# Kernel optimization log

Measured on AMD Instinct MI355X. Metric: run time of the kernel, lower is better.

## Reference

```python
import jax, jax.numpy as jnp
import numpy as np

B, N, NODE, EDGE, H, SK, SV, PK, PV = 1, 512, 256, 128, 8, 16, 16, 4, 4
EPS = 1e-8
SCALAR_SCALE = (3 * SK) ** -0.5          # num_attn_logits=3
POINT_SCALE = (3 * PK * (9.0 / 2.0)) ** -0.5
PAIR_SCALE = 3 ** -0.5


def setup_inputs() -> dict:
    key = jax.random.key(0)
    ks = jax.random.split(key, 16)
    s = 0.02
    return {
        "node": jax.random.normal(ks[0], (B, N, NODE), jnp.float32),
        "edge": jax.random.normal(ks[1], (B, N, N, EDGE), jnp.float32),
        "rotations": jax.random.normal(ks[2], (B, N, 3, 3), jnp.float32),
        "translations": jax.random.normal(ks[3], (B, N, 3), jnp.float32),
        "W_sq": jax.random.normal(ks[4], (NODE, H * SK), jnp.float32) * s,
        "W_sk": jax.random.normal(ks[5], (NODE, H * SK), jnp.float32) * s,
        "W_sv": jax.random.normal(ks[6], (NODE, H * SV), jnp.float32) * s,
        "W_pq": jax.random.normal(ks[7], (NODE, H * PK * 3), jnp.float32) * s,
        "W_pk": jax.random.normal(ks[8], (NODE, H * PK * 3), jnp.float32) * s,
        "W_pv": jax.random.normal(ks[9], (NODE, H * PV * 3), jnp.float32) * s,
        "point_weights": jnp.log(jnp.expm1(jnp.ones((H,), jnp.float32))),  # softplus^-1(1)
        "W_pb": jax.random.normal(ks[10], (EDGE, H), jnp.float32) * s,
        "b_pb": jnp.zeros((H,), jnp.float32),
        "W_out": jax.random.normal(ks[11], (H * (SV + EDGE + PV * 4), NODE), jnp.float32) * s,
        "b_out": jnp.zeros((NODE,), jnp.float32),
    }


def reference(node, edge, rotations, translations, W_sq, W_sk, W_sv, W_pq, W_pk, W_pv,
              point_weights, W_pb, b_pb, W_out, b_out):
    b, n, _ = node.shape
    # scalar q/k/v: (b, n, h, d)
    qs = (node @ W_sq).reshape(b, n, H, SK)
    ks_ = (node @ W_sk).reshape(b, n, H, SK)
    vs = (node @ W_sv).reshape(b, n, H, SV)
    # point q/k/v in local frame: (b, n, h, d, 3) -> rotate + translate into global frame
    t = translations[:, :, None, None, :]  # (b, n, 1, 1, 3)
    qp = jnp.einsum('bnhdc,bnrc->bnhdr', (node @ W_pq).reshape(b, n, H, PK, 3), rotations) + t
    kp = jnp.einsum('bnhdc,bnrc->bnhdr', (node @ W_pk).reshape(b, n, H, PK, 3), rotations) + t
    vp = jnp.einsum('bnhdc,bnrc->bnhdr', (node @ W_pv).reshape(b, n, H, PV, 3), rotations) + t

    # scalar logits (b, h, i, j)
    logits_scalar = jnp.einsum('bihd,bjhd->bhij', qs, ks_) * SCALAR_SCALE
    # pairwise bias (b, h, i, j)
    logits_pair = (jnp.einsum('bijd,dh->bhij', edge, W_pb) + b_pb[None, :, None, None]) * PAIR_SCALE
    # point logits: sum_{d,c} ||q - k||^2 via expansion (avoids (b,i,j,h,d,3) tensor)
    q2 = (qp ** 2).sum((-2, -1)).transpose(0, 2, 1)  # (b, h, i)
    k2 = (kp ** 2).sum((-2, -1)).transpose(0, 2, 1)  # (b, h, j)
    cross = jnp.einsum('bihdc,bjhdc->bhij', qp, kp)
    point_dist = q2[:, :, :, None] + k2[:, :, None, :] - 2.0 * cross  # (b, h, i, j)
    pw = jax.nn.softplus(point_weights)[None, :, None, None]  # (1, h, 1, 1)
    logits_points = -0.5 * (point_dist * pw * POINT_SCALE)

    attn = jax.nn.softmax(logits_scalar + logits_points + logits_pair, axis=-1)  # (b, h, i, j)

    res_scalar = jnp.einsum('bhij,bjhd->bihd', attn, vs).reshape(b, n, H * SV)
    res_pair = jnp.einsum('bhij,bijd->bihd', attn, edge).reshape(b, n, H * EDGE)
    res_pts = jnp.einsum('bhij,bjhdr->bihdr', attn, vp) - t  # back to origin
    res_pts = jnp.einsum('bnhdr,bnrc->bnhdc', res_pts, rotations)  # inverse rotation (R^T)
    res_norm = jnp.sqrt((res_pts ** 2).sum(-1) + EPS)  # (b, n, h, d)

    out = jnp.concatenate([
        res_scalar,
        res_pts.reshape(b, n, H * PV * 3),
        res_norm.reshape(b, n, H * PV),
        res_pair,
    ], axis=-1)
    return out @ W_out + b_out
```

## Files before the change

### kernel.cpp

```cpp
#include <hip/hip_runtime.h>
#include <hip/hip_fp16.h>
#include <math.h>

#define NN 512
#define NODE_D 256
#define EDGE_D 128
#define HN 8

#define SCALAR_SCALE 0.14433756729740643f
#define POINT_SCALE  0.13608276348795434f
#define PAIR_SCALE   0.5773502691896258f

#define OFF_QS   0
#define OFF_KS   65536
#define OFF_VS   131072
#define OFF_VP   196608
#define OFF_QCAT 245760
#define OFF_KCAT 393216
#define OFF_FEAT 540672
#define OFF_PRAW OFF_FEAT
#define OFF_LG16 1196032
#define OFF_OUTP 2244608

__global__ __launch_bounds__(256) void k_projgemm(
    const float* __restrict__ node,
    const float* __restrict__ Wsq, const float* __restrict__ Wsk, const float* __restrict__ Wsv,
    const float* __restrict__ Wpq, const float* __restrict__ Wpk, const float* __restrict__ Wpv,
    float* __restrict__ ws)
{
  __shared__ float As[32 * 33];
  __shared__ float Bs[32 * 36];
  const int t = threadIdx.x;
  const int it = blockIdx.x;
  const int ct = blockIdx.y;

  const float* W; int ncol, col0; float* dst; int ldd, dcol0;
  if (ct < 12) {
    int a = ct >> 2;
    W = (a == 0) ? Wsq : (a == 1) ? Wsk : Wsv;
    ncol = 128; col0 = (ct & 3) * 32;
    dst = ws + ((a == 0) ? OFF_QS : (a == 1) ? OFF_KS : OFF_VS);
    ldd = 128; dcol0 = col0;
  } else {
    int p = ct - 12;
    int a = p / 3, cc = p % 3;
    W = (a == 0) ? Wpq : (a == 1) ? Wpk : Wpv;
    ncol = 96; col0 = cc * 32;
    dst = ws + OFF_PRAW;
    ldd = 288; dcol0 = a * 96 + cc * 32;
  }

  const int row = t & 31, cb = (t >> 5) * 4;
  float4 acc = {0.f, 0.f, 0.f, 0.f};

  for (int kt = 0; kt < 8; ++kt) {
    __syncthreads();
    #pragma unroll
    for (int q = 0; q < 4; ++q) {
      int f = t + q * 256; int r = f >> 5, c = f & 31;
      As[r * 33 + c] = node[(size_t)(it * 32 + r) * 256 + kt * 32 + c];
      Bs[r * 36 + c] = W[(size_t)(kt * 32 + r) * ncol + col0 + c];
    }
    __syncthreads();
    #pragma unroll
    for (int k = 0; k < 32; ++k) {
      float a = As[row * 33 + k];
      float4 b = *(const float4*)&Bs[k * 36 + cb];
      acc.x += a * b.x; acc.y += a * b.y; acc.z += a * b.z; acc.w += a * b.w;
    }
  }
  *(float4*)&dst[(size_t)(it * 32 + row) * ldd + dcol0 + cb] = acc;
}

__global__ __launch_bounds__(256) void k_rot2(
    const float* __restrict__ rotm, const float* __restrict__ trans,
    const float* __restrict__ pw_in, const float* __restrict__ bpb,
    float* __restrict__ ws)
{
  __shared__ float p_l[4][288];
  __shared__ float r_l[4][288];
  __shared__ float q2_l[4][8];
  __shared__ float k2_l[4][8];
  __shared__ float pw_l[8];
  __shared__ float bpb_l[8];
  const int t = threadIdx.x;
  const int n0 = blockIdx.x * 4;
  const float* praw = ws + OFF_PRAW;
  const float* qs_g = ws + OFF_QS;
  const float* ks_g = ws + OFF_KS;

  if (t < 8) {
    float x = pw_in[t];
    pw_l[t] = 0.5f * POINT_SCALE * logf(1.0f + expf(x));
    bpb_l[t] = bpb[t];
  }
  for (int idx = t; idx < 1152; idx += 256) {
    int row = idx / 288, rem = idx % 288;
    p_l[row][rem] = praw[(size_t)(n0 + row) * 288 + rem];
  }
  __syncthreads();

  for (int idx = t; idx < 1152; idx += 256) {
    int row = idx / 288, rem = idx % 288;
    int a = rem / 96, col = rem % 96;
    int rr = col % 3;
    int n = n0 + row;
    const float* R = rotm + (size_t)(n * 3 + rr) * 3;
    const float* P = &p_l[row][a * 96 + (col - rr)];
    float val = P[0] * R[0] + P[1] * R[1] + P[2] * R[2] + trans[n * 3 + rr];
    r_l[row][a * 96 + col] = val;
    if (a == 2) (ws + OFF_VP)[(size_t)n * 96 + col] = val;
  }
  __syncthreads();

  if (t < 64) {
    int row = t >> 4, rem = t & 15;
    int which = rem >> 3, h = rem & 7;
    const float* src = &r_l[row][which * 96 + h * 12];
    float s = 0.f;
    #pragma unroll
    for (int m = 0; m < 12; ++m) s += src[m] * src[m];
    if (which == 0) q2_l[row][h] = s; else k2_l[row][h] = s;
  }
  __syncthreads();

  for (int idx = t; idx < 2304; idx += 256) {
    int side = idx >= 1152;
    int per = idx - side * 1152;
    int row = per / 288, s = per % 288;
    int h = s / 36, e = s % 36;
    int n = n0 + row;
    float val;
    if (!side) {
      val = (e < 16) ? qs_g[(size_t)n * 128 + h * 16 + e] * SCALAR_SCALE
          : (e < 28) ? 2.0f * pw_l[h] * r_l[row][h * 12 + (e - 16)]
          : (e == 32) ? -pw_l[h]
          : (e == 33) ? (bpb_l[h] * PAIR_SCALE - pw_l[h] * q2_l[row][h])
          : 0.f;
      (ws + OFF_QCAT)[(size_t)n * 288 + s] = val;
    } else {
      val = (e < 16) ? ks_g[(size_t)n * 128 + h * 16 + e]
          : (e < 28) ? r_l[row][96 + h * 12 + (e - 16)]
          : (e == 32) ? k2_l[row][h]
          : (e == 33) ? 1.f
          : 0.f;
      (ws + OFF_KCAT)[(size_t)n * 288 + s] = val;
    }
  }
}

__global__ __launch_bounds__(256) void k_S(
    const float* __restrict__ ws_c, __half* __restrict__ lg16)
{
  __shared__ float4 Qt[32 * 36];
  __shared__ float4 Kt[32 * 37];
  __shared__ __half lgst[32 * 32 * 8];
  const int t = threadIdx.x;
  const int it = blockIdx.x, jt = blockIdx.y;
  const float* Qc = ws_c + OFF_QCAT;
  const float* Kc = ws_c + OFF_KCAT;
  const int ti = t >> 4, tj = t & 15;

  for (int hg = 0; hg < 2; ++hg) {
    __syncthreads();
    for (int f = t; f < 1152; f += 256) {
      int row = f / 36, c = f % 36;
      Qt[row * 36 + c] = *(const float4*)&Qc[(size_t)(it * 32 + row) * 288 + hg * 144 + c * 4];
      Kt[row * 37 + c] = *(const float4*)&Kc[(size_t)(jt * 32 + row) * 288 + hg * 144 + c * 4];
    }
    __syncthreads();

    float acc[2][2][4];
    #pragma unroll
    for (int a = 0; a < 2; ++a)
      #pragma unroll
      for (int b = 0; b < 2; ++b)
        #pragma unroll
        for (int h = 0; h < 4; ++h) acc[a][b][h] = 0.f;

    for (int c = 0; c < 9; ++c) {
      #pragma unroll
      for (int hh = 0; hh < 4; ++hh) {
        float4 q0 = Qt[(2 * ti + 0) * 36 + hh * 9 + c];
        float4 q1 = Qt[(2 * ti + 1) * 36 + hh * 9 + c];
        float4 k0 = Kt[(2 * tj + 0) * 37 + hh * 9 + c];
        float4 k1 = Kt[(2 * tj + 1) * 37 + hh * 9 + c];
        acc[0][0][hh] += q0.x * k0.x + q0.y * k0.y + q0.z * k0.z + q0.w * k0.w;
        acc[0][1][hh] += q0.x * k1.x + q0.y * k1.y + q0.z * k1.z + q0.w * k1.w;
        acc[1][0][hh] += q1.x * k0.x + q1.y * k0.y + q1.z * k0.z + q1.w * k0.w;
        acc[1][1][hh] += q1.x * k1.x + q1.y * k1.y + q1.z * k1.z + q1.w * k1.w;
      }
    }
    #pragma unroll
    for (int a = 0; a < 2; ++a)
      #pragma unroll
      for (int b = 0; b < 2; ++b)
        #pragma unroll
        for (int hh = 0; hh < 4; ++hh)
          lgst[((2 * ti + a) * 32 + (2 * tj + b)) * 8 + hg * 4 + hh] = __float2half(acc[a][b][hh]);
  }
  __syncthreads();

  for (int f = t; f < 1024; f += 256) {
    int il = f >> 5, jl = f & 31;
    float4 v = *(const float4*)&lgst[(il * 32 + jl) * 8];
    *(float4*)&lg16[((size_t)(it * 32 + il) * 512 + jt * 32 + jl) * 8] = v;
  }
}

static __device__ inline __half2 shfl_xor_h2(__half2 h, int m) {
  int v = __builtin_bit_cast(int, h);
  v = __shfl_xor(v, m);
  return __builtin_bit_cast(__half2, v);
}

__global__ __launch_bounds__(256) void k_pair(
    const float* __restrict__ edge, const float* __restrict__ Wpb,
    __half* __restrict__ lg16)
{
  const int t = threadIdx.x;
  const int jt = blockIdx.x, i = blockIdx.y;
  const int l = t & 63, w = t >> 6;
  const int rg = (l >> 4) & 3, sub = l & 15;

  float wv[4][2][8];
  #pragma unroll
  for (int k = 0; k < 4; ++k)
    #pragma unroll
    for (int c = 0; c < 2; ++c)
      #pragma unroll
      for (int h = 0; h < 8; ++h)
        wv[k][c][h] = Wpb[(size_t)(2 * sub + c + 32 * k) * 8 + h] * PAIR_SCALE;

  for (int p = 0; p < 8; ++p) {
    const int r = p * 16 + w * 4 + rg;
    const int j = jt * 128 + r;
    const float* eptr = edge + ((size_t)i * 512 + j) * 128 + 2 * sub;

    float2 e0 = *(const float2*)(eptr);
    float2 e1 = *(const float2*)(eptr + 32);
    float2 e2 = *(const float2*)(eptr + 64);
    float2 e3 = *(const float2*)(eptr + 96);

    float p8[8];
    #pragma unroll
    for (int h = 0; h < 8; ++h)
      p8[h] = e0.x * wv[0][0][h] + e0.y * wv[0][1][h]
            + e1.x * wv[1][0][h] + e1.y * wv[1][1][h]
            + e2.x * wv[2][0][h] + e2.y * wv[2][1][h]
            + e3.x * wv[3][0][h] + e3.y * wv[3][1][h];

    __half2 h0 = __floats2half2_rn(p8[0], p8[1]);
    __half2 h1 = __floats2half2_rn(p8[2], p8[3]);
    __half2 h2 = __floats2half2_rn(p8[4], p8[5]);
    __half2 h3 = __floats2half2_rn(p8[6], p8[7]);
    #pragma unroll
    for (int m = 1; m <= 8; m <<= 1) {
      h0 = __hadd2(h0, shfl_xor_h2(h0, m));
      h1 = __hadd2(h1, shfl_xor_h2(h1, m));
      h2 = __hadd2(h2, shfl_xor_h2(h2, m));
      h3 = __hadd2(h3, shfl_xor_h2(h3, m));
    }
    if (sub == 0) {
      __half* dst = lg16 + ((size_t)i * 512 + j) * 8;
      float4 cur = *(float4*)dst;
      __half2* ch = (__half2*)&cur;
      ch[0] = __hadd2(ch[0], h0);
      ch[1] = __hadd2(ch[1], h1);
      ch[2] = __hadd2(ch[2], h2);
      ch[3] = __hadd2(ch[3], h3);
      *(float4*)dst = cur;
    }
  }
}

__global__ __launch_bounds__(256) void k_attnout(
    const float* __restrict__ edge, const float* __restrict__ rotm,
    const float* __restrict__ trans, const float* __restrict__ ws,
    const __half* __restrict__ lg16, float* __restrict__ feat)
{
  __shared__ float aw[512 * 12];
  __shared__ float pl[8 * 128 * 8];
  __shared__ float vsp[8 * 128];
  __shared__ float vpp[8 * 96];
  __shared__ float op_l[96];
  __shared__ float rp_l[96];
  __shared__ float linv_l[8];

  const int t = threadIdx.x;
  const int i = blockIdx.x;

  {
    const int lane = t & 63, wid = t >> 6;
    #pragma unroll
    for (int hh = 0; hh < 2; ++hh) {
      int h = wid * 2 + hh;
      float x[8];
      float m = -1e30f;
      #pragma unroll
      for (int r = 0; r < 8; ++r) {
        int j = lane + r * 64;
        x[r] = __half2float(lg16[((size_t)i * 512 + j) * 8 + h]);
        m = fmaxf(m, x[r]);
      }
      #pragma unroll
      for (int s = 32; s; s >>= 1) m = fmaxf(m, __shfl_xor(m, s));
      float ssum = 0.f;
      #pragma unroll
      for (int r = 0; r < 8; ++r) {
        float pv = __expf(x[r] - m);
        ssum += pv;
        aw[(lane + r * 64) * 12 + h] = pv;
      }
      #pragma unroll
      for (int s = 32; s; s >>= 1) ssum += __shfl_xor(ssum, s);
      if (lane == 0) linv_l[h] = 1.0f / ssum;
    }
  }
  __syncthreads();

  const int dq = t & 31, js = t >> 5;
  const int b = dq >> 4;
  const int c0 = dq, c1 = dq + 32, c2 = dq + 64;
  const int h0 = c0 / 12, h1 = c1 / 12, h2 = c2 / 12;

  float4 aclo[4], achi[4];
  #pragma unroll
  for (int k = 0; k < 4; ++k) { aclo[k] = {0,0,0,0}; achi[k] = {0,0,0,0}; }
  float avs[4] = {0,0,0,0};
  float avp[3] = {0,0,0};

  const float* ebase = edge + (size_t)i * 512 * 128;
  const float* vsg = ws + OFF_VS;
  const float* vpg = ws + OFF_VP;

  for (int jj = 0; jj < 64; ++jj) {
    int j = js * 64 + jj;
    const float* er = ebase + (size_t)j * 128 + dq;
    const float* vr = vsg + (size_t)j * 128 + dq;
    const float* pr = vpg + (size_t)j * 96;
    float4 wlo = *(const float4*)&aw[j * 12];
    float4 whi = *(const float4*)&aw[j * 12 + 4];
    #pragma unroll
    for (int k = 0; k < 4; ++k) {
      float e = er[32 * k];
      aclo[k].x += wlo.x * e; aclo[k].y += wlo.y * e;
      aclo[k].z += wlo.z * e; aclo[k].w += wlo.w * e;
      achi[k].x += whi.x * e; achi[k].y += whi.y * e;
      achi[k].z += whi.z * e; achi[k].w += whi.w * e;
      float vv = vr[32 * k];
      float wk = (k == 0) ? (b ? wlo.y : wlo.x)
               : (k == 1) ? (b ? wlo.w : wlo.z)
               : (k == 2) ? (b ? whi.y : whi.x)
               :            (b ? whi.w : whi.z);
      avs[k] += wk * vv;
    }
    avp[0] += aw[j * 12 + h0] * pr[c0];
    avp[1] += aw[j * 12 + h1] * pr[c1];
    avp[2] += aw[j * 12 + h2] * pr[c2];
  }

  #pragma unroll
  for (int k = 0; k < 4; ++k) {
    int d = dq + 32 * k;
    *(float4*)&pl[(js * 128 + d) * 8] = aclo[k];
    *(float4*)&pl[(js * 128 + d) * 8 + 4] = achi[k];
    vsp[js * 128 + d] = avs[k];
  }
  vpp[js * 96 + c0] = avp[0];
  vpp[js * 96 + c1] = avp[1];
  vpp[js * 96 + c2] = avp[2];
  __syncthreads();

  float* frow = feat + (size_t)i * 1280;

  {
    int d = t >> 1, hq = (t & 1) * 4;
    float4 s = {0,0,0,0};
    #pragma unroll
    for (int q = 0; q < 8; ++q) {
      float4 v = *(const float4*)&pl[(q * 128 + d) * 8 + hq];
      s.x += v.x; s.y += v.y; s.z += v.z; s.w += v.w;
    }
    frow[256 + (hq + 0) * 128 + d] = s.x * linv_l[hq + 0];
    frow[256 + (hq + 1) * 128 + d] = s.y * linv_l[hq + 1];
    frow[256 + (hq + 2) * 128 + d] = s.z * linv_l[hq + 2];
    frow[256 + (hq + 3) * 128 + d] = s.w * linv_l[hq + 3];
  }
  if (t < 128) {
    float s = 0.f;
    #pragma unroll
    for (int q = 0; q < 8; ++q) s += vsp[q * 128 + t];
    frow[t] = s * linv_l[t >> 4];
  }
  if (t < 96) {
    float s = 0.f;
    #pragma unroll
    for (int q = 0; q < 8; ++q) s += vpp[q * 96 + t];
    op_l[t] = s * linv_l[t / 12] - trans[i * 3 + (t % 3)];
  }
  __syncthreads();

  if (t < 96) {
    int c = t % 3, base = t - c;
    const float* R = rotm + (size_t)i * 9;
    float val = op_l[base] * R[c] + op_l[base + 1] * R[3 + c] + op_l[base + 2] * R[6 + c];
    rp_l[t] = val;
    frow[128 + t] = val;
  }
  __syncthreads();
  if (t < 32) {
    float x = rp_l[t * 3], y = rp_l[t * 3 + 1], z = rp_l[t * 3 + 2];
    frow[224 + t] = sqrtf(x * x + y * y + z * z + 1e-8f);
  }
}

__global__ __launch_bounds__(256) void k_outp(
    const float* __restrict__ feat, const float* __restrict__ Wout,
    float* __restrict__ ws)
{
  __shared__ float As[32 * 33];
  __shared__ float Bs[32 * 36];
  const int t = threadIdx.x;
  const int it = blockIdx.x, ot = blockIdx.y, z = blockIdx.z;
  const int row = t & 31, cb = (t >> 5) * 4;
  float4 acc = {0.f, 0.f, 0.f, 0.f};

  for (int kk = 0; kk < 10; ++kk) {
    int kt = z * 10 + kk;
    __syncthreads();
    #pragma unroll
    for (int q = 0; q < 4; ++q) {
      int f = t + q * 256; int r = f >> 5, c = f & 31;
      As[r * 33 + c] = feat[(size_t)(it * 32 + r) * 1280 + kt * 32 + c];
      Bs[r * 36 + c] = Wout[(size_t)(kt * 32 + r) * 256 + ot * 32 + c];
    }
    __syncthreads();
    #pragma unroll
    for (int k = 0; k < 32; ++k) {
      float a = As[row * 33 + k];
      float4 bv = *(const float4*)&Bs[k * 36 + cb];
      acc.x += a * bv.x; acc.y += a * bv.y; acc.z += a * bv.z; acc.w += a * bv.w;
    }
  }
  float* pc = ws + OFF_OUTP + (size_t)z * 131072;
  *(float4*)&pc[(size_t)(it * 32 + row) * 256 + ot * 32 + cb] = acc;
}

__global__ __launch_bounds__(256) void k_outr(
    const float* __restrict__ ws, const float* __restrict__ bout,
    float* __restrict__ out)
{
  const int q = blockIdx.x * 256 + threadIdx.x;
  const float* pc = ws + OFF_OUTP;
  float4 a = *(const float4*)&pc[(size_t)q * 4];
  float4 b = *(const float4*)&pc[(size_t)q * 4 + 131072];
  float4 c = *(const float4*)&pc[(size_t)q * 4 + 262144];
  float4 d = *(const float4*)&pc[(size_t)q * 4 + 393216];
  float4 bias = *(const float4*)&bout[(q & 63) * 4];
  float4 r;
  r.x = a.x + b.x + c.x + d.x + bias.x;
  r.y = a.y + b.y + c.y + d.y + bias.y;
  r.z = a.z + b.z + c.z + d.z + bias.z;
  r.w = a.w + b.w + c.w + d.w + bias.w;
  *(float4*)&out[(size_t)q * 4] = r;
}

extern "C" void kernel_launch(void* const* d_in, const int* in_sizes, int n_in,
                              void* d_out, int out_size, void* d_ws, size_t ws_size,
                              hipStream_t stream) {
  const float* node  = (const float*)d_in[0];
  const float* edge  = (const float*)d_in[1];
  const float* rotm  = (const float*)d_in[2];
  const float* trans = (const float*)d_in[3];
  const float* Wsq   = (const float*)d_in[4];
  const float* Wsk   = (const float*)d_in[5];
  const float* Wsv   = (const float*)d_in[6];
  const float* Wpq   = (const float*)d_in[7];
  const float* Wpk   = (const float*)d_in[8];
  const float* Wpv   = (const float*)d_in[9];
  const float* pw    = (const float*)d_in[10];
  const float* Wpb   = (const float*)d_in[11];
  const float* bpb   = (const float*)d_in[12];
  const float* Wout  = (const float*)d_in[13];
  const float* bout  = (const float*)d_in[14];
  float* ws   = (float*)d_ws;
  float* out  = (float*)d_out;
  float* feat = ws + OFF_FEAT;
  __half* lg16 = (__half*)(ws + OFF_LG16);

  k_projgemm<<<dim3(16, 21), 256, 0, stream>>>(node, Wsq, Wsk, Wsv, Wpq, Wpk, Wpv, ws);
  k_rot2<<<128, 256, 0, stream>>>(rotm, trans, pw, bpb, ws);
  k_S<<<dim3(16, 16), 256, 0, stream>>>(ws, lg16);
  k_pair<<<dim3(4, 512), 256, 0, stream>>>(edge, Wpb, lg16);
  k_attnout<<<512, 256, 0, stream>>>(edge, rotm, trans, ws, lg16, feat);
  k_outp<<<dim3(16, 8, 4), 256, 0, stream>>>(feat, Wout, ws);
  k_outr<<<128, 256, 0, stream>>>(ws, bout, out);
}
```

Baseline: 114.1 us.

## Split attention-output kernel into softmax, edge-pair reduction, and reduce kernels

The fused attention-output kernel, which streamed each row's 256 KB of edge data through a single 512-block grid, is split in three. The first kernel computes the softmax and writes normalized weights to the workspace. The second reads edge data with float4 loads over a 4x512 grid and produces partial sums per j-tile, and the third reduces those partials into feat. The aim is more parallelism and wider loads on the bandwidth-bound edge pass, at the cost of two extra launches and extra workspace traffic for the weights and partials.

```diff
diff --git a/kernel.cpp b/kernel.cpp
--- a/kernel.cpp
+++ b/kernel.cpp
@@ -20,7 +20,9 @@
 #define OFF_FEAT 540672
 #define OFF_PRAW OFF_FEAT
 #define OFF_LG16 1196032
-#define OFF_OUTP 2244608
+#define OFF_W    2244608
+#define OFF_RP   4341760
+#define OFF_OUTP 6438912
 
 __global__ __launch_bounds__(256) void k_projgemm(
     const float* __restrict__ node,
@@ -274,13 +276,12 @@
   }
 }
 
-__global__ __launch_bounds__(256) void k_attnout(
-    const float* __restrict__ edge, const float* __restrict__ rotm,
-    const float* __restrict__ trans, const float* __restrict__ ws,
-    const __half* __restrict__ lg16, float* __restrict__ feat)
+__global__ __launch_bounds__(256) void k_soft(
+    const float* __restrict__ rotm, const float* __restrict__ trans,
+    const float* __restrict__ ws_r, const __half* __restrict__ lg16,
+    float* __restrict__ wout, float* __restrict__ feat)
 {
   __shared__ float aw[512 * 12];
-  __shared__ float pl[8 * 128 * 8];
   __shared__ float vsp[8 * 128];
   __shared__ float vpp[8 * 96];
   __shared__ float op_l[96];
@@ -319,35 +320,36 @@
   }
   __syncthreads();
 
+  {
+    float4 l0 = *(const float4*)&linv_l[0];
+    float4 l1 = *(const float4*)&linv_l[4];
+    for (int f = t; f < 1024; f += 256) {
+      int j = f >> 1, q = f & 1;
+      float4 v = *(const float4*)&aw[j * 12 + q * 4];
+      float4 lv = q ? l1 : l0;
+      v.x *= lv.x; v.y *= lv.y; v.z *= lv.z; v.w *= lv.w;
+      *(float4*)&wout[((size_t)i * 512 + j) * 8 + q * 4] = v;
+    }
+  }
+
   const int dq = t & 31, js = t >> 5;
-  const int b = dq >> 4;
   const int c0 = dq, c1 = dq + 32, c2 = dq + 64;
   const int h0 = c0 / 12, h1 = c1 / 12, h2 = c2 / 12;
-
-  float4 aclo[4], achi[4];
-  #pragma unroll
-  for (int k = 0; k < 4; ++k) { aclo[k] = {0,0,0,0}; achi[k] = {0,0,0,0}; }
+  const int b = dq >> 4;
+
   float avs[4] = {0,0,0,0};
   float avp[3] = {0,0,0};
-
-  const float* ebase = edge + (size_t)i * 512 * 128;
-  const float* vsg = ws + OFF_VS;
-  const float* vpg = ws + OFF_VP;
+  const float* vsg = ws_r + OFF_VS;
+  const float* vpg = ws_r + OFF_VP;
 
   for (int jj = 0; jj < 64; ++jj) {
     int j = js * 64 + jj;
-    const float* er = ebase + (size_t)j * 128 + dq;
     const float* vr = vsg + (size_t)j * 128 + dq;
     const float* pr = vpg + (size_t)j * 96;
     float4 wlo = *(const float4*)&aw[j * 12];
     float4 whi = *(const float4*)&aw[j * 12 + 4];
     #pragma unroll
     for (int k = 0; k < 4; ++k) {
-      float e = er[32 * k];
-      aclo[k].x += wlo.x * e; aclo[k].y += wlo.y * e;
-      aclo[k].z += wlo.z * e; aclo[k].w += wlo.w * e;
-      achi[k].x += whi.x * e; achi[k].y += whi.y * e;
-      achi[k].z += whi.z * e; achi[k].w += whi.w * e;
       float vv = vr[32 * k];
       float wk = (k == 0) ? (b ? wlo.y : wlo.x)
                : (k == 1) ? (b ? wlo.w : wlo.z)
@@ -361,12 +363,7 @@
   }
 
   #pragma unroll
-  for (int k = 0; k < 4; ++k) {
-    int d = dq + 32 * k;
-    *(float4*)&pl[(js * 128 + d) * 8] = aclo[k];
-    *(float4*)&pl[(js * 128 + d) * 8 + 4] = achi[k];
-    vsp[js * 128 + d] = avs[k];
-  }
+  for (int k = 0; k < 4; ++k) vsp[js * 128 + dq + 32 * k] = avs[k];
   vpp[js * 96 + c0] = avp[0];
   vpp[js * 96 + c1] = avp[1];
   vpp[js * 96 + c2] = avp[2];
@@ -374,19 +371,6 @@
 
   float* frow = feat + (size_t)i * 1280;
 
-  {
-    int d = t >> 1, hq = (t & 1) * 4;
-    float4 s = {0,0,0,0};
-    #pragma unroll
-    for (int q = 0; q < 8; ++q) {
-      float4 v = *(const float4*)&pl[(q * 128 + d) * 8 + hq];
-      s.x += v.x; s.y += v.y; s.z += v.z; s.w += v.w;
-    }
-    frow[256 + (hq + 0) * 128 + d] = s.x * linv_l[hq + 0];
-    frow[256 + (hq + 1) * 128 + d] = s.y * linv_l[hq + 1];
-    frow[256 + (hq + 2) * 128 + d] = s.z * linv_l[hq + 2];
-    frow[256 + (hq + 3) * 128 + d] = s.w * linv_l[hq + 3];
-  }
   if (t < 128) {
     float s = 0.f;
     #pragma unroll
@@ -413,6 +397,66 @@
     float x = rp_l[t * 3], y = rp_l[t * 3 + 1], z = rp_l[t * 3 + 2];
     frow[224 + t] = sqrtf(x * x + y * y + z * z + 1e-8f);
   }
+}
+
+#define FMA4(A, S, E) { A.x += (S)*(E).x; A.y += (S)*(E).y; A.z += (S)*(E).z; A.w += (S)*(E).w; }
+
+__global__ __launch_bounds__(256) void k_rpair(
+    const float* __restrict__ edge, const float* __restrict__ ws_r,
+    float* __restrict__ ws_w)
+{
+  __shared__ float4 pl[8][8][32];
+  const int t = threadIdx.x;
+  const int jt = blockIdx.x, i = blockIdx.y;
+  const int dq = t & 31, g = t >> 5;
+
+  const float* eb = edge + ((size_t)i * 512 + jt * 128) * 128;
+  const float* wb = ws_r + OFF_W + ((size_t)i * 512 + jt * 128) * 8;
+
+  float4 acc[8];
+  #pragma unroll
+  for (int h = 0; h < 8; ++h) acc[h] = {0.f, 0.f, 0.f, 0.f};
+
+  for (int r = 0; r < 16; ++r) {
+    int j = g * 16 + r;
+    float4 e = *(const float4*)&eb[(size_t)j * 128 + dq * 4];
+    float4 w0 = *(const float4*)&wb[j * 8];
+    float4 w1 = *(const float4*)&wb[j * 8 + 4];
+    FMA4(acc[0], w0.x, e); FMA4(acc[1], w0.y, e);
+    FMA4(acc[2], w0.z, e); FMA4(acc[3], w0.w, e);
+    FMA4(acc[4], w1.x, e); FMA4(acc[5], w1.y, e);
+    FMA4(acc[6], w1.z, e); FMA4(acc[7], w1.w, e);
+  }
+  #pragma unroll
+  for (int h = 0; h < 8; ++h) pl[g][h][dq] = acc[h];
+  __syncthreads();
+
+  {
+    const int h = t >> 5;
+    float4 s = {0.f, 0.f, 0.f, 0.f};
+    #pragma unroll
+    for (int q = 0; q < 8; ++q) {
+      float4 v = pl[q][h][dq];
+      s.x += v.x; s.y += v.y; s.z += v.z; s.w += v.w;
+    }
+    float* dst = ws_w + OFF_RP + (size_t)(i * 4 + jt) * 1024 + h * 128 + dq * 4;
+    *(float4*)dst = s;
+  }
+}
+
+__global__ __launch_bounds__(256) void k_rpred(
+    const float* __restrict__ ws_r, float* __restrict__ feat)
+{
+  const int t = threadIdx.x, i = blockIdx.x;
+  const int dq = t & 31, h = t >> 5;
+  const float* rp = ws_r + OFF_RP + (size_t)i * 4096;
+  float4 s = {0.f, 0.f, 0.f, 0.f};
+  #pragma unroll
+  for (int q = 0; q < 4; ++q) {
+    float4 v = *(const float4*)&rp[q * 1024 + h * 128 + dq * 4];
+    s.x += v.x; s.y += v.y; s.z += v.z; s.w += v.w;
+  }
+  *(float4*)&feat[(size_t)i * 1280 + 256 + h * 128 + dq * 4] = s;
 }
 
 __global__ __launch_bounds__(256) void k_outp(
@@ -493,7 +537,9 @@
   k_rot2<<<128, 256, 0, stream>>>(rotm, trans, pw, bpb, ws);
   k_S<<<dim3(16, 16), 256, 0, stream>>>(ws, lg16);
   k_pair<<<dim3(4, 512), 256, 0, stream>>>(edge, Wpb, lg16);
-  k_attnout<<<512, 256, 0, stream>>>(edge, rotm, trans, ws, lg16, feat);
+  k_soft<<<512, 256, 0, stream>>>(rotm, trans, ws, lg16, ws + OFF_W, feat);
+  k_rpair<<<dim3(4, 512), 256, 0, stream>>>(edge, ws, ws);
+  k_rpred<<<512, 256, 0, stream>>>(ws, feat);
   k_outp<<<dim3(16, 8, 4), 256, 0, stream>>>(feat, Wout, ws);
   k_outr<<<128, 256, 0, stream>>>(ws, bout, out);
 }
```

Measured after the change: 129.5 us. 13.5% more time.

## Cache fp16 copy of edge tensor in pair kernel and read it in attention output

Applied to the files above, without the earlier changes.

The pair-bias kernel now also converts the edge tensor to fp16 and writes it to workspace. The attention-output kernel then reads this half-size copy instead of the fp32 edge. The attention-output accumulation is also restructured to use vectorized per-thread loads and a head-major weight layout. The intent is to cut edge read bandwidth in the second pass. The cost is an extra large write and reduced precision in the pair feature.

```diff
diff --git a/kernel.cpp b/kernel.cpp
--- a/kernel.cpp
+++ b/kernel.cpp
@@ -11,16 +11,17 @@
 #define POINT_SCALE  0.13608276348795434f
 #define PAIR_SCALE   0.5773502691896258f
 
-#define OFF_QS   0
-#define OFF_KS   65536
-#define OFF_VS   131072
-#define OFF_VP   196608
-#define OFF_QCAT 245760
-#define OFF_KCAT 393216
-#define OFF_FEAT 540672
-#define OFF_PRAW OFF_FEAT
-#define OFF_LG16 1196032
-#define OFF_OUTP 2244608
+#define OFF_QS     0
+#define OFF_KS     65536
+#define OFF_VS     131072
+#define OFF_VP     196608
+#define OFF_QCAT   245760
+#define OFF_KCAT   393216
+#define OFF_FEAT   540672
+#define OFF_PRAW   OFF_FEAT
+#define OFF_LG16   1196032
+#define OFF_EDGE16 2244608
+#define OFF_OUTP   19021824
 
 __global__ __launch_bounds__(256) void k_projgemm(
     const float* __restrict__ node,
@@ -214,41 +215,44 @@
   return __builtin_bit_cast(__half2, v);
 }
 
-__global__ __launch_bounds__(256) void k_pair(
+__global__ __launch_bounds__(256) void k_pair16(
     const float* __restrict__ edge, const float* __restrict__ Wpb,
-    __half* __restrict__ lg16)
+    __half* __restrict__ lg16, __half* __restrict__ edge16)
 {
   const int t = threadIdx.x;
   const int jt = blockIdx.x, i = blockIdx.y;
   const int l = t & 63, w = t >> 6;
   const int rg = (l >> 4) & 3, sub = l & 15;
 
-  float wv[4][2][8];
+  float wv[8][8];
   #pragma unroll
-  for (int k = 0; k < 4; ++k)
-    #pragma unroll
-    for (int c = 0; c < 2; ++c)
-      #pragma unroll
-      for (int h = 0; h < 8; ++h)
-        wv[k][c][h] = Wpb[(size_t)(2 * sub + c + 32 * k) * 8 + h] * PAIR_SCALE;
+  for (int dd = 0; dd < 8; ++dd)
+    #pragma unroll
+    for (int h = 0; h < 8; ++h)
+      wv[dd][h] = Wpb[(size_t)(8 * sub + dd) * 8 + h] * PAIR_SCALE;
 
   for (int p = 0; p < 8; ++p) {
     const int r = p * 16 + w * 4 + rg;
     const int j = jt * 128 + r;
-    const float* eptr = edge + ((size_t)i * 512 + j) * 128 + 2 * sub;
-
-    float2 e0 = *(const float2*)(eptr);
-    float2 e1 = *(const float2*)(eptr + 32);
-    float2 e2 = *(const float2*)(eptr + 64);
-    float2 e3 = *(const float2*)(eptr + 96);
-
+    const float4* e4 = (const float4*)(edge + ((size_t)i * 512 + j) * 128 + 8 * sub);
+    float4 a = e4[0], b = e4[1];
+
+    float4 pk;
+    ((__half2*)&pk)[0] = __floats2half2_rn(a.x, a.y);
+    ((__half2*)&pk)[1] = __floats2half2_rn(a.z, a.w);
+    ((__half2*)&pk)[2] = __floats2half2_rn(b.x, b.y);
+    ((__half2*)&pk)[3] = __floats2half2_rn(b.z, b.w);
+    *(float4*)(edge16 + ((size_t)i * 512 + j) * 128 + 8 * sub) = pk;
+
+    float e[8] = {a.x, a.y, a.z, a.w, b.x, b.y, b.z, b.w};
     float p8[8];
     #pragma unroll
-    for (int h = 0; h < 8; ++h)
-      p8[h] = e0.x * wv[0][0][h] + e0.y * wv[0][1][h]
-            + e1.x * wv[1][0][h] + e1.y * wv[1][1][h]
-            + e2.x * wv[2][0][h] + e2.y * wv[2][1][h]
-            + e3.x * wv[3][0][h] + e3.y * wv[3][1][h];
+    for (int h = 0; h < 8; ++h) {
+      float s = 0.f;
+      #pragma unroll
+      for (int dd = 0; dd < 8; ++dd) s += e[dd] * wv[dd][h];
+      p8[h] = s;
+    }
 
     __half2 h0 = __floats2half2_rn(p8[0], p8[1]);
     __half2 h1 = __floats2half2_rn(p8[2], p8[3]);
@@ -275,14 +279,12 @@
 }
 
 __global__ __launch_bounds__(256) void k_attnout(
-    const float* __restrict__ edge, const float* __restrict__ rotm,
-    const float* __restrict__ trans, const float* __restrict__ ws,
+    const __half* __restrict__ edge16, const float* __restrict__ rotm,
+    const float* __restrict__ trans, const float* __restrict__ ws_r,
     const __half* __restrict__ lg16, float* __restrict__ feat)
 {
-  __shared__ float aw[512 * 12];
-  __shared__ float pl[8 * 128 * 8];
-  __shared__ float vsp[8 * 128];
-  __shared__ float vpp[8 * 96];
+  __shared__ float awu[8 * 512];
+  __shared__ float pl[8][8][128];
   __shared__ float op_l[96];
   __shared__ float rp_l[96];
   __shared__ float linv_l[8];
@@ -310,7 +312,7 @@
       for (int r = 0; r < 8; ++r) {
         float pv = __expf(x[r] - m);
         ssum += pv;
-        aw[(lane + r * 64) * 12 + h] = pv;
+        awu[h * 512 + lane + r * 64] = pv;
       }
       #pragma unroll
       for (int s = 32; s; s >>= 1) ssum += __shfl_xor(ssum, s);
@@ -320,72 +322,83 @@
   __syncthreads();
 
   const int dq = t & 31, js = t >> 5;
-  const int b = dq >> 4;
-  const int c0 = dq, c1 = dq + 32, c2 = dq + 64;
-  const int h0 = c0 / 12, h1 = c1 / 12, h2 = c2 / 12;
-
-  float4 aclo[4], achi[4];
+  const int hvs = dq >> 2;
+  const int hvp = dq / 3;
+
+  float acc[8][4];
   #pragma unroll
-  for (int k = 0; k < 4; ++k) { aclo[k] = {0,0,0,0}; achi[k] = {0,0,0,0}; }
-  float avs[4] = {0,0,0,0};
-  float avp[3] = {0,0,0};
-
-  const float* ebase = edge + (size_t)i * 512 * 128;
-  const float* vsg = ws + OFF_VS;
-  const float* vpg = ws + OFF_VP;
+  for (int h = 0; h < 8; ++h)
+    #pragma unroll
+    for (int e = 0; e < 4; ++e) acc[h][e] = 0.f;
+  float avs[4] = {0, 0, 0, 0};
+  float avp[4] = {0, 0, 0, 0};
+
+  const float* vsg = ws_r + OFF_VS;
+  const float* vpg = ws_r + OFF_VP;
 
   for (int jj = 0; jj < 64; ++jj) {
     int j = js * 64 + jj;
-    const float* er = ebase + (size_t)j * 128 + dq;
-    const float* vr = vsg + (size_t)j * 128 + dq;
-    const float* pr = vpg + (size_t)j * 96;
-    float4 wlo = *(const float4*)&aw[j * 12];
-    float4 whi = *(const float4*)&aw[j * 12 + 4];
-    #pragma unroll
-    for (int k = 0; k < 4; ++k) {
-      float e = er[32 * k];
-      aclo[k].x += wlo.x * e; aclo[k].y += wlo.y * e;
-      aclo[k].z += wlo.z * e; aclo[k].w += wlo.w * e;
-      achi[k].x += whi.x * e; achi[k].y += whi.y * e;
-      achi[k].z += whi.z * e; achi[k].w += whi.w * e;
-      float vv = vr[32 * k];
-      float wk = (k == 0) ? (b ? wlo.y : wlo.x)
-               : (k == 1) ? (b ? wlo.w : wlo.z)
-               : (k == 2) ? (b ? whi.y : whi.x)
-               :            (b ? whi.w : whi.z);
-      avs[k] += wk * vv;
-    }
-    avp[0] += aw[j * 12 + h0] * pr[c0];
-    avp[1] += aw[j * 12 + h1] * pr[c1];
-    avp[2] += aw[j * 12 + h2] * pr[c2];
+    uint2 ev = *(const uint2*)(edge16 + ((size_t)i * 512 + j) * 128 + dq * 4);
+    __half2 e01 = __builtin_bit_cast(__half2, ev.x);
+    __half2 e23 = __builtin_bit_cast(__half2, ev.y);
+    float e0 = __low2float(e01), e1 = __high2float(e01);
+    float e2 = __low2float(e23), e3 = __high2float(e23);
+
+    float wgt[8];
+    #pragma unroll
+    for (int h = 0; h < 8; ++h) wgt[h] = awu[h * 512 + j];
+
+    #pragma unroll
+    for (int h = 0; h < 8; ++h) {
+      acc[h][0] += wgt[h] * e0; acc[h][1] += wgt[h] * e1;
+      acc[h][2] += wgt[h] * e2; acc[h][3] += wgt[h] * e3;
+    }
+
+    float4 v = *(const float4*)&vsg[(size_t)j * 128 + dq * 4];
+    float wv_ = wgt[hvs];
+    avs[0] += wv_ * v.x; avs[1] += wv_ * v.y;
+    avs[2] += wv_ * v.z; avs[3] += wv_ * v.w;
+
+    if (dq < 24) {
+      float4 pv4 = *(const float4*)&vpg[(size_t)j * 96 + dq * 4];
+      float wp_ = wgt[hvp];
+      avp[0] += wp_ * pv4.x; avp[1] += wp_ * pv4.y;
+      avp[2] += wp_ * pv4.z; avp[3] += wp_ * pv4.w;
+    }
   }
 
   #pragma unroll
-  for (int k = 0; k < 4; ++k) {
-    int d = dq + 32 * k;
-    *(float4*)&pl[(js * 128 + d) * 8] = aclo[k];
-    *(float4*)&pl[(js * 128 + d) * 8 + 4] = achi[k];
-    vsp[js * 128 + d] = avs[k];
-  }
-  vpp[js * 96 + c0] = avp[0];
-  vpp[js * 96 + c1] = avp[1];
-  vpp[js * 96 + c2] = avp[2];
+  for (int h = 0; h < 8; ++h) {
+    float4 pv = {acc[h][0], acc[h][1], acc[h][2], acc[h][3]};
+    *(float4*)&pl[js][h][dq * 4] = pv;
+  }
+  __syncthreads();
+
+  float* vsp = awu;
+  float* vpp = awu + 1024;
+  {
+    float4 sv = {avs[0], avs[1], avs[2], avs[3]};
+    *(float4*)&vsp[js * 128 + dq * 4] = sv;
+    if (dq < 24) {
+      float4 pv = {avp[0], avp[1], avp[2], avp[3]};
+      *(float4*)&vpp[js * 96 + dq * 4] = pv;
+    }
+  }
   __syncthreads();
 
   float* frow = feat + (size_t)i * 1280;
 
   {
-    int d = t >> 1, hq = (t & 1) * 4;
-    float4 s = {0,0,0,0};
+    const int h = t >> 5, d4 = (t & 31) * 4;
+    float4 s = {0, 0, 0, 0};
     #pragma unroll
     for (int q = 0; q < 8; ++q) {
-      float4 v = *(const float4*)&pl[(q * 128 + d) * 8 + hq];
+      float4 v = *(const float4*)&pl[q][h][d4];
       s.x += v.x; s.y += v.y; s.z += v.z; s.w += v.w;
     }
-    frow[256 + (hq + 0) * 128 + d] = s.x * linv_l[hq + 0];
-    frow[256 + (hq + 1) * 128 + d] = s.y * linv_l[hq + 1];
-    frow[256 + (hq + 2) * 128 + d] = s.z * linv_l[hq + 2];
-    frow[256 + (hq + 3) * 128 + d] = s.w * linv_l[hq + 3];
+    float li = linv_l[h];
+    s.x *= li; s.y *= li; s.z *= li; s.w *= li;
+    *(float4*)&frow[256 + h * 128 + d4] = s;
   }
   if (t < 128) {
     float s = 0.f;
@@ -487,13 +500,14 @@
   float* ws   = (float*)d_ws;
   float* out  = (float*)d_out;
   float* feat = ws + OFF_FEAT;
-  __half* lg16 = (__half*)(ws + OFF_LG16);
+  __half* lg16   = (__half*)(ws + OFF_LG16);
+  __half* edge16 = (__half*)(ws + OFF_EDGE16);
 
   k_projgemm<<<dim3(16, 21), 256, 0, stream>>>(node, Wsq, Wsk, Wsv, Wpq, Wpk, Wpv, ws);
   k_rot2<<<128, 256, 0, stream>>>(rotm, trans, pw, bpb, ws);
   k_S<<<dim3(16, 16), 256, 0, stream>>>(ws, lg16);
-  k_pair<<<dim3(4, 512), 256, 0, stream>>>(edge, Wpb, lg16);
-  k_attnout<<<512, 256, 0, stream>>>(edge, rotm, trans, ws, lg16, feat);
+  k_pair16<<<dim3(4, 512), 256, 0, stream>>>(edge, Wpb, lg16, edge16);
+  k_attnout<<<512, 256, 0, stream>>>(edge16, rotm, trans, ws, lg16, feat);
   k_outp<<<dim3(16, 8, 4), 256, 0, stream>>>(feat, Wout, ws);
   k_outr<<<128, 256, 0, stream>>>(ws, bout, out);
 }
```

New measurement: 127.1 us. 1.11x slower.

## Fuse pair-bias and attention-output kernels with fp16 edge row staged in LDS

Applied to the files above, without the earlier changes.

Merges the pair-bias kernel and the attention-output kernel into one 512-thread block per query row. The block loads that row's edge tensor once, converts it to fp16 and stores it in a swizzled LDS buffer, then reuses it for both the pair logits and the attention-weighted edge sum. The intent is to read the 32 MB edge tensor from HBM once instead of twice and to drop the read-modify-write of the logits buffer. In exchange it uses about 128 KB of LDS per block, which limits occupancy, and it lowers edge precision to fp16 for both uses.

```diff
diff --git a/kernel.cpp b/kernel.cpp
--- a/kernel.cpp
+++ b/kernel.cpp
@@ -208,196 +208,151 @@
   }
 }
 
-static __device__ inline __half2 shfl_xor_h2(__half2 h, int m) {
-  int v = __builtin_bit_cast(int, h);
-  v = __shfl_xor(v, m);
-  return __builtin_bit_cast(__half2, v);
-}
-
-__global__ __launch_bounds__(256) void k_pair(
-    const float* __restrict__ edge, const float* __restrict__ Wpb,
-    __half* __restrict__ lg16)
-{
+__global__ __launch_bounds__(512) void k_fused(
+    const float* __restrict__ edge, const float* __restrict__ rotm,
+    const float* __restrict__ trans, const float* __restrict__ ws_r,
+    const __half* __restrict__ lg16, const float* __restrict__ Wpb,
+    float* __restrict__ feat)
+{
+  __shared__ __half e16[512 * 128];
+  __shared__ __half awl[8 * 520];
+  __shared__ float wpb_l[128 * 8];
+  __shared__ float linv_l[8];
+  __shared__ float vsp[4 * 128];
+  __shared__ float vpp[4 * 96];
+  __shared__ float op_l[96];
+  __shared__ float rp_l[96];
+
   const int t = threadIdx.x;
-  const int jt = blockIdx.x, i = blockIdx.y;
-  const int l = t & 63, w = t >> 6;
-  const int rg = (l >> 4) & 3, sub = l & 15;
-
-  float wv[4][2][8];
-  #pragma unroll
-  for (int k = 0; k < 4; ++k)
-    #pragma unroll
-    for (int c = 0; c < 2; ++c)
+  const int i = blockIdx.x;
+
+  for (int f = t; f < 1024; f += 512) wpb_l[f] = Wpb[f] * PAIR_SCALE;
+
+  {
+    const float4* src = (const float4*)(edge + (size_t)i * 512 * 128);
+    #pragma unroll 8
+    for (int r = 0; r < 32; ++r) {
+      int idx = r * 512 + t;
+      int j = idx >> 5, c = idx & 31;
+      float4 v = src[idx];
+      int p = c ^ (j & 31);
+      __half2* dst = (__half2*)&e16[j * 128 + p * 4];
+      dst[0] = __floats2half2_rn(v.x, v.y);
+      dst[1] = __floats2half2_rn(v.z, v.w);
+    }
+  }
+  __syncthreads();
+
+  {
+    float p8[8] = {0, 0, 0, 0, 0, 0, 0, 0};
+    #pragma unroll 4
+    for (int c = 0; c < 32; ++c) {
+      int p = c ^ (t & 31);
+      __half2 ea = *(__half2*)&e16[t * 128 + p * 4];
+      __half2 eb = *(__half2*)&e16[t * 128 + p * 4 + 2];
+      float e0 = __low2float(ea), e1 = __high2float(ea);
+      float e2 = __low2float(eb), e3 = __high2float(eb);
+      const float* w0 = &wpb_l[(c * 4 + 0) * 8];
+      const float* w1 = &wpb_l[(c * 4 + 1) * 8];
+      const float* w2 = &wpb_l[(c * 4 + 2) * 8];
+      const float* w3 = &wpb_l[(c * 4 + 3) * 8];
       #pragma unroll
       for (int h = 0; h < 8; ++h)
-        wv[k][c][h] = Wpb[(size_t)(2 * sub + c + 32 * k) * 8 + h] * PAIR_SCALE;
-
-  for (int p = 0; p < 8; ++p) {
-    const int r = p * 16 + w * 4 + rg;
-    const int j = jt * 128 + r;
-    const float* eptr = edge + ((size_t)i * 512 + j) * 128 + 2 * sub;
-
-    float2 e0 = *(const float2*)(eptr);
-    float2 e1 = *(const float2*)(eptr + 32);
-    float2 e2 = *(const float2*)(eptr + 64);
-    float2 e3 = *(const float2*)(eptr + 96);
-
-    float p8[8];
-    #pragma unroll
-    for (int h = 0; h < 8; ++h)
-      p8[h] = e0.x * wv[0][0][h] + e0.y * wv[0][1][h]
-            + e1.x * wv[1][0][h] + e1.y * wv[1][1][h]
-            + e2.x * wv[2][0][h] + e2.y * wv[2][1][h]
-            + e3.x * wv[3][0][h] + e3.y * wv[3][1][h];
-
-    __half2 h0 = __floats2half2_rn(p8[0], p8[1]);
-    __half2 h1 = __floats2half2_rn(p8[2], p8[3]);
-    __half2 h2 = __floats2half2_rn(p8[4], p8[5]);
-    __half2 h3 = __floats2half2_rn(p8[6], p8[7]);
-    #pragma unroll
-    for (int m = 1; m <= 8; m <<= 1) {
-      h0 = __hadd2(h0, shfl_xor_h2(h0, m));
-      h1 = __hadd2(h1, shfl_xor_h2(h1, m));
-      h2 = __hadd2(h2, shfl_xor_h2(h2, m));
-      h3 = __hadd2(h3, shfl_xor_h2(h3, m));
-    }
-    if (sub == 0) {
-      __half* dst = lg16 + ((size_t)i * 512 + j) * 8;
-      float4 cur = *(float4*)dst;
-      __half2* ch = (__half2*)&cur;
-      ch[0] = __hadd2(ch[0], h0);
-      ch[1] = __hadd2(ch[1], h1);
-      ch[2] = __hadd2(ch[2], h2);
-      ch[3] = __hadd2(ch[3], h3);
-      *(float4*)dst = cur;
-    }
-  }
-}
-
-__global__ __launch_bounds__(256) void k_attnout(
-    const float* __restrict__ edge, const float* __restrict__ rotm,
-    const float* __restrict__ trans, const float* __restrict__ ws,
-    const __half* __restrict__ lg16, float* __restrict__ feat)
-{
-  __shared__ float aw[512 * 12];
-  __shared__ float pl[8 * 128 * 8];
-  __shared__ float vsp[8 * 128];
-  __shared__ float vpp[8 * 96];
-  __shared__ float op_l[96];
-  __shared__ float rp_l[96];
-  __shared__ float linv_l[8];
-
-  const int t = threadIdx.x;
-  const int i = blockIdx.x;
+        p8[h] += e0 * w0[h] + e1 * w1[h] + e2 * w2[h] + e3 * w3[h];
+    }
+    float4 lv = *(const float4*)(lg16 + ((size_t)i * 512 + t) * 8);
+    const __half2* lh = (const __half2*)&lv;
+    #pragma unroll
+    for (int h = 0; h < 8; ++h) {
+      float base = (h & 1) ? __high2float(lh[h >> 1]) : __low2float(lh[h >> 1]);
+      awl[h * 520 + t] = __float2half(p8[h] + base);
+    }
+  }
+  __syncthreads();
 
   {
-    const int lane = t & 63, wid = t >> 6;
-    #pragma unroll
-    for (int hh = 0; hh < 2; ++hh) {
-      int h = wid * 2 + hh;
-      float x[8];
-      float m = -1e30f;
-      #pragma unroll
-      for (int r = 0; r < 8; ++r) {
-        int j = lane + r * 64;
-        x[r] = __half2float(lg16[((size_t)i * 512 + j) * 8 + h]);
-        m = fmaxf(m, x[r]);
-      }
-      #pragma unroll
-      for (int s = 32; s; s >>= 1) m = fmaxf(m, __shfl_xor(m, s));
-      float ssum = 0.f;
-      #pragma unroll
-      for (int r = 0; r < 8; ++r) {
-        float pv = __expf(x[r] - m);
-        ssum += pv;
-        aw[(lane + r * 64) * 12 + h] = pv;
-      }
-      #pragma unroll
-      for (int s = 32; s; s >>= 1) ssum += __shfl_xor(ssum, s);
-      if (lane == 0) linv_l[h] = 1.0f / ssum;
-    }
-  }
-  __syncthreads();
-
-  const int dq = t & 31, js = t >> 5;
-  const int b = dq >> 4;
-  const int c0 = dq, c1 = dq + 32, c2 = dq + 64;
-  const int h0 = c0 / 12, h1 = c1 / 12, h2 = c2 / 12;
-
-  float4 aclo[4], achi[4];
-  #pragma unroll
-  for (int k = 0; k < 4; ++k) { aclo[k] = {0,0,0,0}; achi[k] = {0,0,0,0}; }
-  float avs[4] = {0,0,0,0};
-  float avp[3] = {0,0,0};
-
-  const float* ebase = edge + (size_t)i * 512 * 128;
-  const float* vsg = ws + OFF_VS;
-  const float* vpg = ws + OFF_VP;
-
-  for (int jj = 0; jj < 64; ++jj) {
-    int j = js * 64 + jj;
-    const float* er = ebase + (size_t)j * 128 + dq;
-    const float* vr = vsg + (size_t)j * 128 + dq;
-    const float* pr = vpg + (size_t)j * 96;
-    float4 wlo = *(const float4*)&aw[j * 12];
-    float4 whi = *(const float4*)&aw[j * 12 + 4];
-    #pragma unroll
-    for (int k = 0; k < 4; ++k) {
-      float e = er[32 * k];
-      aclo[k].x += wlo.x * e; aclo[k].y += wlo.y * e;
-      aclo[k].z += wlo.z * e; aclo[k].w += wlo.w * e;
-      achi[k].x += whi.x * e; achi[k].y += whi.y * e;
-      achi[k].z += whi.z * e; achi[k].w += whi.w * e;
-      float vv = vr[32 * k];
-      float wk = (k == 0) ? (b ? wlo.y : wlo.x)
-               : (k == 1) ? (b ? wlo.w : wlo.z)
-               : (k == 2) ? (b ? whi.y : whi.x)
-               :            (b ? whi.w : whi.z);
-      avs[k] += wk * vv;
-    }
-    avp[0] += aw[j * 12 + h0] * pr[c0];
-    avp[1] += aw[j * 12 + h1] * pr[c1];
-    avp[2] += aw[j * 12 + h2] * pr[c2];
-  }
-
-  #pragma unroll
-  for (int k = 0; k < 4; ++k) {
-    int d = dq + 32 * k;
-    *(float4*)&pl[(js * 128 + d) * 8] = aclo[k];
-    *(float4*)&pl[(js * 128 + d) * 8 + 4] = achi[k];
-    vsp[js * 128 + d] = avs[k];
-  }
-  vpp[js * 96 + c0] = avp[0];
-  vpp[js * 96 + c1] = avp[1];
-  vpp[js * 96 + c2] = avp[2];
+    const int w = t >> 6, lane = t & 63;
+    float x[8];
+    float m = -1e30f;
+    #pragma unroll
+    for (int r = 0; r < 8; ++r) {
+      x[r] = __half2float(awl[w * 520 + lane + r * 64]);
+      m = fmaxf(m, x[r]);
+    }
+    #pragma unroll
+    for (int s = 32; s; s >>= 1) m = fmaxf(m, __shfl_xor(m, s));
+    float ssum = 0.f;
+    #pragma unroll
+    for (int r = 0; r < 8; ++r) {
+      float pv = __expf(x[r] - m);
+      ssum += pv;
+      awl[w * 520 + lane + r * 64] = __float2half(pv);
+    }
+    #pragma unroll
+    for (int s = 32; s; s >>= 1) ssum += __shfl_xor(ssum, s);
+    if (lane == 0) linv_l[w] = 1.0f / ssum;
+  }
   __syncthreads();
 
   float* frow = feat + (size_t)i * 1280;
 
   {
-    int d = t >> 1, hq = (t & 1) * 4;
-    float4 s = {0,0,0,0};
-    #pragma unroll
-    for (int q = 0; q < 8; ++q) {
-      float4 v = *(const float4*)&pl[(q * 128 + d) * 8 + hq];
-      s.x += v.x; s.y += v.y; s.z += v.z; s.w += v.w;
-    }
-    frow[256 + (hq + 0) * 128 + d] = s.x * linv_l[hq + 0];
-    frow[256 + (hq + 1) * 128 + d] = s.y * linv_l[hq + 1];
-    frow[256 + (hq + 2) * 128 + d] = s.z * linv_l[hq + 2];
-    frow[256 + (hq + 3) * 128 + d] = s.w * linv_l[hq + 3];
-  }
+    const int w = t >> 6, l = t & 63;
+    const int dq = l & 31, jh = l >> 5;
+    float a0 = 0.f, a1 = 0.f, a2 = 0.f, a3 = 0.f;
+    #pragma unroll 4
+    for (int jj = 0; jj < 256; ++jj) {
+      int j = jh * 256 + jj;
+      float wgt = __half2float(awl[w * 520 + j]);
+      int p = dq ^ (j & 31);
+      __half2 ea = *(__half2*)&e16[j * 128 + p * 4];
+      __half2 eb = *(__half2*)&e16[j * 128 + p * 4 + 2];
+      a0 += wgt * __low2float(ea); a1 += wgt * __high2float(ea);
+      a2 += wgt * __low2float(eb); a3 += wgt * __high2float(eb);
+    }
+    a0 += __shfl_down(a0, 32); a1 += __shfl_down(a1, 32);
+    a2 += __shfl_down(a2, 32); a3 += __shfl_down(a3, 32);
+    if (l < 32) {
+      float li = linv_l[w];
+      float4 o = {a0 * li, a1 * li, a2 * li, a3 * li};
+      *(float4*)&frow[256 + w * 128 + dq * 4] = o;
+    }
+  }
+
+  {
+    const int c = t & 127, jq = t >> 7;
+    const int h = c >> 4;
+    const float* vsg = ws_r + OFF_VS;
+    float acc = 0.f;
+    #pragma unroll 4
+    for (int jj = 0; jj < 128; ++jj) {
+      int j = jq * 128 + jj;
+      acc += __half2float(awl[h * 520 + j]) * vsg[(size_t)j * 128 + c];
+    }
+    vsp[jq * 128 + c] = acc;
+  }
+  if (t < 384) {
+    const int c = t % 96, jq = t / 96;
+    const int h = c / 12;
+    const float* vpg = ws_r + OFF_VP;
+    float acc = 0.f;
+    #pragma unroll 4
+    for (int jj = 0; jj < 128; ++jj) {
+      int j = jq * 128 + jj;
+      acc += __half2float(awl[h * 520 + j]) * vpg[(size_t)j * 96 + c];
+    }
+    vpp[jq * 96 + c] = acc;
+  }
+  __syncthreads();
+
   if (t < 128) {
-    float s = 0.f;
-    #pragma unroll
-    for (int q = 0; q < 8; ++q) s += vsp[q * 128 + t];
+    float s = vsp[t] + vsp[128 + t] + vsp[256 + t] + vsp[384 + t];
     frow[t] = s * linv_l[t >> 4];
   }
-  if (t < 96) {
-    float s = 0.f;
-    #pragma unroll
-    for (int q = 0; q < 8; ++q) s += vpp[q * 96 + t];
-    op_l[t] = s * linv_l[t / 12] - trans[i * 3 + (t % 3)];
+  if (t >= 256 && t < 352) {
+    int u = t - 256;
+    float s = vpp[u] + vpp[96 + u] + vpp[192 + u] + vpp[288 + u];
+    op_l[u] = s * linv_l[u / 12] - trans[i * 3 + (u % 3)];
   }
   __syncthreads();
 
@@ -492,8 +447,7 @@
   k_projgemm<<<dim3(16, 21), 256, 0, stream>>>(node, Wsq, Wsk, Wsv, Wpq, Wpk, Wpv, ws);
   k_rot2<<<128, 256, 0, stream>>>(rotm, trans, pw, bpb, ws);
   k_S<<<dim3(16, 16), 256, 0, stream>>>(ws, lg16);
-  k_pair<<<dim3(4, 512), 256, 0, stream>>>(edge, Wpb, lg16);
-  k_attnout<<<512, 256, 0, stream>>>(edge, rotm, trans, ws, lg16, feat);
+  k_fused<<<512, 512, 0, stream>>>(edge, rotm, trans, ws, lg16, Wpb, feat);
   k_outp<<<dim3(16, 8, 4), 256, 0, stream>>>(feat, Wout, ws);
   k_outr<<<128, 256, 0, stream>>>(ws, bout, out);
 }
```

Result: slower. 145.2 us (+27.2%).
